# Performance work log

Measured on AMD Instinct MI355X. Metric: run time of the kernel, lower is better.

## Reference

```python
import jax, jax.numpy as jnp
import numpy as np

TEMPERATURE = 0.1
NSAMPLE = 32
B, N_PER, M_PER, C_FEAT = 2, 16384, 4096, 64


def setup_inputs() -> dict:
    key = jax.random.key(0)
    ks = jax.random.split(key, 4)
    xyz = jax.random.normal(ks[0], (B * N_PER, 3), jnp.float32)
    new_xyz = jax.random.normal(ks[1], (B * M_PER, 3), jnp.float32)
    new_xyz_r = jax.random.uniform(ks[2], (B * M_PER, 1), jnp.float32, minval=0.5, maxval=1.0)
    features = jax.random.normal(ks[3], (B * N_PER, C_FEAT), jnp.float32)
    xyz_batch_cnt = jnp.full((B,), N_PER, jnp.int32)
    new_xyz_batch_cnt = jnp.full((B,), M_PER, jnp.int32)
    temperature_decay = jnp.ones((1,), jnp.float32)
    return dict(xyz=xyz, xyz_batch_cnt=xyz_batch_cnt, new_xyz=new_xyz,
                new_xyz_r=new_xyz_r, new_xyz_batch_cnt=new_xyz_batch_cnt,
                features=features, temperature_decay=temperature_decay)


def _ball_query(xyz_b, new_xyz_b, r_b, nsample):
    # xyz_b: (B,N,3), new_xyz_b: (B,M,3), r_b: (B,M)
    # Returns idx (B,M,nsample) int32 (batch-local point indices, first-in-order
    # within the ball, remaining slots filled with first hit, 0 if empty) and
    # empty mask (B,M) bool. Mirrors the CUDA ball_query_deform kernel.
    N = xyz_b.shape[1]
    d2 = jnp.sum((new_xyz_b[:, :, None, :] - xyz_b[:, None, :, :]) ** 2, axis=-1)  # (B,M,N)
    within = d2 < (r_b ** 2)[..., None]
    # key = point index if within radius else N; top_k of -key gives the first
    # nsample in-ball indices in ascending index order.
    key = jnp.where(within, jnp.arange(N, dtype=jnp.int32), jnp.int32(N))
    neg_vals, _ = jax.lax.top_k(-key, nsample)
    cand = -neg_vals  # (B,M,nsample)
    cnt = within.sum(axis=-1)  # (B,M)
    slot_valid = jnp.arange(nsample) < cnt[..., None]
    idx = jnp.where(slot_valid, cand, cand[..., :1])  # pad with first found index
    empty = cnt == 0
    idx = jnp.where(empty[..., None], 0, idx)
    return idx.astype(jnp.int32), empty


def reference(xyz, xyz_batch_cnt, new_xyz, new_xyz_r, new_xyz_batch_cnt, features, temperature_decay):
    b = xyz_batch_cnt.shape[0]
    n = xyz.shape[0] // b
    m = new_xyz.shape[0] // b
    c = features.shape[1]
    real_t = TEMPERATURE * temperature_decay[0]
    explore_r = new_xyz_r + real_t * 5.0  # (M_tot, 1)

    xyz_b = xyz.reshape(b, n, 3)
    nxyz_b = new_xyz.reshape(b, m, 3)
    idx_b, empty_b = _ball_query(xyz_b, nxyz_b, explore_r.reshape(b, m), NSAMPLE)

    gather = jax.vmap(lambda pts, i: pts[i])  # per-batch gather

    grouped_xyz = gather(xyz_b, idx_b)                 # (B,M,ns,3)
    grouped_xyz = grouped_xyz - nxyz_b[:, :, None, :]  # center
    grouped_xyz = jnp.where(empty_b[:, :, None, None], 0.0, grouped_xyz)
    grouped_xyz = grouped_xyz.reshape(b * m, NSAMPLE, 3).transpose(0, 2, 1)  # (M_tot,3,ns)

    dist_xyz = jnp.sqrt(jnp.sum(grouped_xyz * grouped_xyz, axis=1))  # (M_tot,ns)
    weights = 1.0 - jax.nn.sigmoid((dist_xyz - new_xyz_r) / real_t)  # (M_tot,ns)

    feat_b = features.reshape(b, n, c)
    grouped_feat = gather(feat_b, idx_b)  # (B,M,ns,C)
    grouped_feat = jnp.where(empty_b[:, :, None, None], 0.0, grouped_feat)
    grouped_feat = grouped_feat.reshape(b * m, NSAMPLE, c).transpose(0, 2, 1)  # (M_tot,C,ns)

    new_features = jnp.concatenate([grouped_xyz, grouped_feat], axis=1)  # (M_tot,3+C,ns)
    idx = idx_b.reshape(b * m, NSAMPLE)
    return new_features, weights, idx
```

## Files before the change

### kernel.cpp

```cpp
#include <hip/hip_runtime.h>
#include <math.h>

#define NS 32
#define WPB 4
#define SCAN0 2048
#define TSTRIDE 36

__device__ __forceinline__ void write_query(
    int m, int bb, bool empty, int lane,
    const int* sIdxW, float* sT,
    const float* __restrict__ xyz, const float* __restrict__ new_xyz,
    const float* __restrict__ new_xyz_r, const float* __restrict__ features,
    float real_t, float* __restrict__ out, int N_per, int C, int M_tot)
{
#pragma clang fp contract(off)
    const float* xb = xyz + (size_t)bb * N_per * 3;
    const int    j  = lane & 31;
    const size_t nf_base = (size_t)m * (3 + C) * NS;
    float* wout = out + (size_t)M_tot * (3 + C) * NS;
    float* iout = wout + (size_t)M_tot * NS;

    if (lane < NS) {
        const float qx = new_xyz[(size_t)m * 3 + 0];
        const float qy = new_xyz[(size_t)m * 3 + 1];
        const float qz = new_xyz[(size_t)m * 3 + 2];
        const float r_orig = new_xyz_r[m];
        const int pj = empty ? 0 : sIdxW[j];
        float gx = 0.f, gy = 0.f, gz = 0.f;
        if (!empty) {
            gx = xb[(size_t)pj * 3 + 0] - qx;
            gy = xb[(size_t)pj * 3 + 1] - qy;
            gz = xb[(size_t)pj * 3 + 2] - qz;
        }
        float d2 = gx * gx;
        d2 = d2 + gy * gy;
        d2 = d2 + gz * gz;
        float dist = sqrtf(d2);
        float wt = 1.0f / (1.0f + expf((dist - r_orig) / real_t));
        out[nf_base + 0 * NS + j] = gx;
        out[nf_base + 1 * NS + j] = gy;
        out[nf_base + 2 * NS + j] = gz;
        wout[(size_t)m * NS + j] = wt;
        iout[(size_t)m * NS + j] = (float)pj;
    }

    const float* fb = features + (size_t)bb * N_per * C;
    int c0 = 0;
    for (; c0 + 32 <= C; c0 += 32) {
        const int k  = lane & 7;
        const int f4 = 4 * (k & 3);
        #pragma unroll
        for (int t = 0; t < 4; ++t) {
            const int r  = 8 * t + (lane >> 3);
            const int pj = empty ? 0 : sIdxW[r];
            float4 v = make_float4(0.f, 0.f, 0.f, 0.f);
            if (!empty) v = *(const float4*)(fb + (size_t)pj * C + c0 + 4 * k);
            const int rs = r ^ f4;
            sT[(4 * k + 0) * TSTRIDE + rs] = v.x;
            sT[(4 * k + 1) * TSTRIDE + rs] = v.y;
            sT[(4 * k + 2) * TSTRIDE + rs] = v.z;
            sT[(4 * k + 3) * TSTRIDE + rs] = v.w;
        }
        const int jg = lane & 7;
        #pragma unroll
        for (int s2 = 0; s2 < 4; ++s2) {
            const int ch = 8 * s2 + (lane >> 3);
            const int jb = (4 * jg) ^ (4 * ((ch >> 2) & 3));
            float4 w = *(const float4*)&sT[ch * TSTRIDE + jb];
            *(float4*)&out[nf_base + (size_t)(3 + c0 + ch) * NS + 4 * jg] = w;
        }
    }
    if (c0 < C) {
        const int h  = lane >> 5;
        const int pj = empty ? 0 : sIdxW[j];
        const float* frow = fb + (size_t)pj * C;
        for (int c = c0 + h; c < C; c += 2) {
            float v = empty ? 0.f : frow[c];
            out[nf_base + (size_t)(3 + c) * NS + j] = v;
        }
    }
}

__global__ __launch_bounds__(256) void qgd_AC(
    const float* __restrict__ xyz, const float* __restrict__ new_xyz,
    const float* __restrict__ new_xyz_r, const float* __restrict__ features,
    const float* __restrict__ tdec, float* __restrict__ out,
    int* __restrict__ counter, int* __restrict__ list,
    int N_per, int M_per, int C, int M_tot)
{
#pragma clang fp contract(off)
    __shared__ __align__(16) float sBuf[WPB * 32 * TSTRIDE];
    __shared__ int sIdx[WPB][NS];

    const int lane = threadIdx.x & 63;
    const int wv   = threadIdx.x >> 6;
    const int m    = blockIdx.x * WPB + wv;
    if (m >= M_tot) return;

    const int bb = m / M_per;
    const float* xb = xyz + (size_t)bb * N_per * 3;
    const float qx = new_xyz[(size_t)m * 3 + 0];
    const float qy = new_xyz[(size_t)m * 3 + 1];
    const float qz = new_xyz[(size_t)m * 3 + 2];
    const float real_t = 0.1f * tdec[0];
    const float er  = new_xyz_r[m] + real_t * 5.0f;
    const float er2 = er * er;
    const unsigned long long lt = (1ull << lane) - 1ull;

    const int scan0 = (SCAN0 < N_per) ? SCAN0 : N_per;
    int cnt = 0;
    for (int base = 0; base < scan0; base += 256) {
        float d2k[4];
        #pragma unroll
        for (int k = 0; k < 4; ++k) {
            int p = base + k * 64 + lane;
            int pc = (p < N_per) ? p : (N_per - 1);
            const float* pp = xb + (size_t)pc * 3;
            float dx = pp[0] - qx, dy = pp[1] - qy, dz = pp[2] - qz;
            float d2 = dx * dx;
            d2 = d2 + dy * dy;
            d2 = d2 + dz * dz;
            d2k[k] = (p < N_per) ? d2 : 1e30f;
        }
        #pragma unroll
        for (int k = 0; k < 4; ++k) {
            bool hit = d2k[k] < er2;
            unsigned long long msk = __ballot(hit);
            if (hit) {
                int slot = cnt + (int)__popcll(msk & lt);
                if (slot < NS) sIdx[wv][slot] = base + k * 64 + lane;
            }
            cnt += (int)__popcll(msk);
        }
        if (cnt >= NS) break;
    }

    if (cnt >= NS) {
        write_query(m, bb, false, lane, sIdx[wv],
                    sBuf + wv * (32 * TSTRIDE),
                    xyz, new_xyz, new_xyz_r, features, real_t, out,
                    N_per, C, M_tot);
    } else if (lane == 0) {
        int pos = atomicAdd(counter, 1);
        list[pos] = m;
    }
}

__global__ __launch_bounds__(256) void qgd_B(
    const float* __restrict__ xyz, const float* __restrict__ new_xyz,
    const float* __restrict__ new_xyz_r, const float* __restrict__ features,
    const float* __restrict__ tdec, float* __restrict__ out,
    const int* __restrict__ counter, const int* __restrict__ list,
    int N_per, int M_per, int C, int M_tot)
{
#pragma clang fp contract(off)
    __shared__ int sH[WPB][NS];
    __shared__ int sC[WPB];
    __shared__ int sM[NS];
    __shared__ int sTot;
    __shared__ __align__(16) float sT[32 * TSTRIDE];

    const int lane = threadIdx.x & 63;
    const int wv   = threadIdx.x >> 6;
    const int nstrag = *counter;
    const unsigned long long lt = (1ull << lane) - 1ull;
    const float real_t = 0.1f * tdec[0];

    for (int it = blockIdx.x; it < nstrag; it += gridDim.x) {
        const int m  = list[it];
        const int bb = m / M_per;
        const float* xb = xyz + (size_t)bb * N_per * 3;
        const float qx = new_xyz[(size_t)m * 3 + 0];
        const float qy = new_xyz[(size_t)m * 3 + 1];
        const float qz = new_xyz[(size_t)m * 3 + 2];
        const float er  = new_xyz_r[m] + real_t * 5.0f;
        const float er2 = er * er;

        const int rb = (int)(((long long)N_per * wv) / WPB);
        const int re = (int)(((long long)N_per * (wv + 1)) / WPB);

        int cnt = 0;
        for (int base = rb; base < re; base += 256) {
            float d2k[4];
            #pragma unroll
            for (int k = 0; k < 4; ++k) {
                int p = base + k * 64 + lane;
                int pc = (p < re) ? p : (re - 1);
                const float* pp = xb + (size_t)pc * 3;
                float dx = pp[0] - qx, dy = pp[1] - qy, dz = pp[2] - qz;
                float d2 = dx * dx;
                d2 = d2 + dy * dy;
                d2 = d2 + dz * dz;
                d2k[k] = (p < re) ? d2 : 1e30f;
            }
            #pragma unroll
            for (int k = 0; k < 4; ++k) {
                bool hit = d2k[k] < er2;
                unsigned long long msk = __ballot(hit);
                if (hit) {
                    int slot = cnt + (int)__popcll(msk & lt);
                    if (slot < NS) sH[wv][slot] = base + k * 64 + lane;
                }
                cnt += (int)__popcll(msk);
            }
            if (cnt >= NS) break;
        }
        if (lane == 0) sC[wv] = (cnt < NS) ? cnt : NS;
        __syncthreads();

        if (threadIdx.x < NS) {
            const int j  = threadIdx.x;
            const int c0 = sC[0], c1 = sC[1], c2 = sC[2], c3 = sC[3];
            const int o1 = c0, o2 = c0 + c1, o3 = o2 + c2;
            const int tot = o3 + c3;
            int v = 0;
            if (j < tot) {
                if      (j >= o3) v = sH[3][j - o3];
                else if (j >= o2) v = sH[2][j - o2];
                else if (j >= o1) v = sH[1][j - o1];
                else              v = sH[0][j];
            }
            int first = 0;
            if      (c0 > 0) first = sH[0][0];
            else if (c1 > 0) first = sH[1][0];
            else if (c2 > 0) first = sH[2][0];
            else if (c3 > 0) first = sH[3][0];
            sM[j] = (tot == 0) ? 0 : ((j < tot) ? v : first);
            if (j == 0) sTot = tot;
        }
        __syncthreads();

        if (wv == 0) {
            write_query(m, bb, (sTot == 0), lane, sM, sT,
                        xyz, new_xyz, new_xyz_r, features, real_t, out,
                        N_per, C, M_tot);
        }
        __syncthreads();
    }
}

extern "C" void kernel_launch(void* const* d_in, const int* in_sizes, int n_in,
                              void* d_out, int out_size, void* d_ws, size_t ws_size,
                              hipStream_t stream) {
    const float* xyz       = (const float*)d_in[0];
    const float* new_xyz   = (const float*)d_in[2];
    const float* new_xyz_r = (const float*)d_in[3];
    const float* features  = (const float*)d_in[5];
    const float* tdec      = (const float*)d_in[6];

    const int B     = in_sizes[1];
    const int N_tot = in_sizes[0] / 3;
    const int M_tot = in_sizes[2] / 3;
    const int C     = in_sizes[5] / N_tot;
    const int N_per = N_tot / B;
    const int M_per = M_tot / B;

    float* out     = (float*)d_out;
    int*   counter = (int*)d_ws;
    int*   list    = (int*)d_ws + 4;

    hipMemsetAsync(counter, 0, sizeof(int), stream);

    const int blocksA = (M_tot + WPB - 1) / WPB;
    qgd_AC<<<blocksA, 256, 0, stream>>>(xyz, new_xyz, new_xyz_r, features,
                                        tdec, out, counter, list,
                                        N_per, M_per, C, M_tot);
    qgd_B<<<512, 256, 0, stream>>>(xyz, new_xyz, new_xyz_r, features,
                                   tdec, out, counter, list,
                                   N_per, M_per, C, M_tot);
}
```

Before: 122.9 us.

## Fuse straggler ball-query pass into main kernel with in-block cooperative rescan

Merges the two-kernel scheme (fast prefix scan plus a straggler list handled by a second kernel) into one kernel. Queries that do not find enough neighbours in the first 2048 points are now finished inside the same block: all four waves split only the remaining points and merge with the prefix hits. This removes the memset, the atomic list, the second launch, and the rescan of the already-scanned prefix. In exchange, a block with stragglers runs them one after another with block-wide syncs, which can leave waves idle and lengthen the tail.

```diff
diff --git a/kernel.cpp b/kernel.cpp
--- a/kernel.cpp
+++ b/kernel.cpp
@@ -81,94 +81,69 @@
     }
 }
 
-__global__ __launch_bounds__(256) void qgd_AC(
+__device__ __forceinline__ int scan_range(
+    const float* __restrict__ xb, float qx, float qy, float qz, float er2,
+    int rb, int re, int lane, unsigned long long lt, int* hits)
+{
+#pragma clang fp contract(off)
+    int cnt = 0;
+    for (int base = rb; base < re; base += 256) {
+        float d2k[4];
+        #pragma unroll
+        for (int k = 0; k < 4; ++k) {
+            int p = base + k * 64 + lane;
+            int pc = (p < re) ? p : (re - 1);
+            const float* pp = xb + (size_t)pc * 3;
+            float dx = pp[0] - qx, dy = pp[1] - qy, dz = pp[2] - qz;
+            float d2 = dx * dx;
+            d2 = d2 + dy * dy;
+            d2 = d2 + dz * dz;
+            d2k[k] = (p < re) ? d2 : 1e30f;
+        }
+        #pragma unroll
+        for (int k = 0; k < 4; ++k) {
+            bool hit = d2k[k] < er2;
+            unsigned long long msk = __ballot(hit);
+            if (hit) {
+                int slot = cnt + (int)__popcll(msk & lt);
+                if (slot < NS) hits[slot] = base + k * 64 + lane;
+            }
+            cnt += (int)__popcll(msk);
+        }
+        if (cnt >= NS) break;
+    }
+    return cnt;
+}
+
+__global__ __launch_bounds__(256) void qgd_F(
     const float* __restrict__ xyz, const float* __restrict__ new_xyz,
     const float* __restrict__ new_xyz_r, const float* __restrict__ features,
     const float* __restrict__ tdec, float* __restrict__ out,
-    int* __restrict__ counter, int* __restrict__ list,
     int N_per, int M_per, int C, int M_tot)
 {
 #pragma clang fp contract(off)
     __shared__ __align__(16) float sBuf[WPB * 32 * TSTRIDE];
     __shared__ int sIdx[WPB][NS];
+    __shared__ int sH[WPB][NS];
+    __shared__ int sCnt[WPB];
+    __shared__ int sStrag[WPB];
+    __shared__ int sC[WPB];
+    __shared__ int sM[NS];
+    __shared__ int sTot;
 
     const int lane = threadIdx.x & 63;
     const int wv   = threadIdx.x >> 6;
     const int m    = blockIdx.x * WPB + wv;
-    if (m >= M_tot) return;
-
-    const int bb = m / M_per;
-    const float* xb = xyz + (size_t)bb * N_per * 3;
-    const float qx = new_xyz[(size_t)m * 3 + 0];
-    const float qy = new_xyz[(size_t)m * 3 + 1];
-    const float qz = new_xyz[(size_t)m * 3 + 2];
+    const bool valid = (m < M_tot);
+
     const float real_t = 0.1f * tdec[0];
-    const float er  = new_xyz_r[m] + real_t * 5.0f;
-    const float er2 = er * er;
     const unsigned long long lt = (1ull << lane) - 1ull;
-
     const int scan0 = (SCAN0 < N_per) ? SCAN0 : N_per;
+
     int cnt = 0;
-    for (int base = 0; base < scan0; base += 256) {
-        float d2k[4];
-        #pragma unroll
-        for (int k = 0; k < 4; ++k) {
-            int p = base + k * 64 + lane;
-            int pc = (p < N_per) ? p : (N_per - 1);
-            const float* pp = xb + (size_t)pc * 3;
-            float dx = pp[0] - qx, dy = pp[1] - qy, dz = pp[2] - qz;
-            float d2 = dx * dx;
-            d2 = d2 + dy * dy;
-            d2 = d2 + dz * dz;
-            d2k[k] = (p < N_per) ? d2 : 1e30f;
-        }
-        #pragma unroll
-        for (int k = 0; k < 4; ++k) {
-            bool hit = d2k[k] < er2;
-            unsigned long long msk = __ballot(hit);
-            if (hit) {
-                int slot = cnt + (int)__popcll(msk & lt);
-                if (slot < NS) sIdx[wv][slot] = base + k * 64 + lane;
-            }
-            cnt += (int)__popcll(msk);
-        }
-        if (cnt >= NS) break;
-    }
-
-    if (cnt >= NS) {
-        write_query(m, bb, false, lane, sIdx[wv],
-                    sBuf + wv * (32 * TSTRIDE),
-                    xyz, new_xyz, new_xyz_r, features, real_t, out,
-                    N_per, C, M_tot);
-    } else if (lane == 0) {
-        int pos = atomicAdd(counter, 1);
-        list[pos] = m;
-    }
-}
-
-__global__ __launch_bounds__(256) void qgd_B(
-    const float* __restrict__ xyz, const float* __restrict__ new_xyz,
-    const float* __restrict__ new_xyz_r, const float* __restrict__ features,
-    const float* __restrict__ tdec, float* __restrict__ out,
-    const int* __restrict__ counter, const int* __restrict__ list,
-    int N_per, int M_per, int C, int M_tot)
-{
-#pragma clang fp contract(off)
-    __shared__ int sH[WPB][NS];
-    __shared__ int sC[WPB];
-    __shared__ int sM[NS];
-    __shared__ int sTot;
-    __shared__ __align__(16) float sT[32 * TSTRIDE];
-
-    const int lane = threadIdx.x & 63;
-    const int wv   = threadIdx.x >> 6;
-    const int nstrag = *counter;
-    const unsigned long long lt = (1ull << lane) - 1ull;
-    const float real_t = 0.1f * tdec[0];
-
-    for (int it = blockIdx.x; it < nstrag; it += gridDim.x) {
-        const int m  = list[it];
-        const int bb = m / M_per;
+    int bb = 0;
+    if (valid) {
+        bb = m / M_per;
         const float* xb = xyz + (size_t)bb * N_per * 3;
         const float qx = new_xyz[(size_t)m * 3 + 0];
         const float qy = new_xyz[(size_t)m * 3 + 1];
@@ -176,62 +151,68 @@
         const float er  = new_xyz_r[m] + real_t * 5.0f;
         const float er2 = er * er;
 
-        const int rb = (int)(((long long)N_per * wv) / WPB);
-        const int re = (int)(((long long)N_per * (wv + 1)) / WPB);
-
-        int cnt = 0;
-        for (int base = rb; base < re; base += 256) {
-            float d2k[4];
-            #pragma unroll
-            for (int k = 0; k < 4; ++k) {
-                int p = base + k * 64 + lane;
-                int pc = (p < re) ? p : (re - 1);
-                const float* pp = xb + (size_t)pc * 3;
-                float dx = pp[0] - qx, dy = pp[1] - qy, dz = pp[2] - qz;
-                float d2 = dx * dx;
-                d2 = d2 + dy * dy;
-                d2 = d2 + dz * dz;
-                d2k[k] = (p < re) ? d2 : 1e30f;
-            }
-            #pragma unroll
-            for (int k = 0; k < 4; ++k) {
-                bool hit = d2k[k] < er2;
-                unsigned long long msk = __ballot(hit);
-                if (hit) {
-                    int slot = cnt + (int)__popcll(msk & lt);
-                    if (slot < NS) sH[wv][slot] = base + k * 64 + lane;
-                }
-                cnt += (int)__popcll(msk);
-            }
-            if (cnt >= NS) break;
-        }
-        if (lane == 0) sC[wv] = (cnt < NS) ? cnt : NS;
+        cnt = scan_range(xb, qx, qy, qz, er2, 0, scan0, lane, lt, sIdx[wv]);
+
+        if (cnt >= NS) {
+            write_query(m, bb, false, lane, sIdx[wv],
+                        sBuf + wv * (32 * TSTRIDE),
+                        xyz, new_xyz, new_xyz_r, features, real_t, out,
+                        N_per, C, M_tot);
+        }
+    }
+    if (lane == 0) {
+        sCnt[wv]   = cnt;
+        sStrag[wv] = (valid && cnt < NS) ? 1 : 0;
+    }
+    __syncthreads();
+
+    for (int s = 0; s < WPB; ++s) {
+        if (!sStrag[s]) continue;
+
+        const int ms  = blockIdx.x * WPB + s;
+        const int bbs = ms / M_per;
+        const float* xbs = xyz + (size_t)bbs * N_per * 3;
+        const float qx = new_xyz[(size_t)ms * 3 + 0];
+        const float qy = new_xyz[(size_t)ms * 3 + 1];
+        const float qz = new_xyz[(size_t)ms * 3 + 2];
+        const float er  = new_xyz_r[ms] + real_t * 5.0f;
+        const float er2 = er * er;
+
+        const int rem = N_per - scan0;
+        const int rb  = scan0 + (int)(((long long)rem * wv) / WPB);
+        const int re  = scan0 + (int)(((long long)rem * (wv + 1)) / WPB);
+
+        int c2 = scan_range(xbs, qx, qy, qz, er2, rb, re, lane, lt, sH[wv]);
+        if (lane == 0) sC[wv] = (c2 < NS) ? c2 : NS;
         __syncthreads();
 
         if (threadIdx.x < NS) {
             const int j  = threadIdx.x;
-            const int c0 = sC[0], c1 = sC[1], c2 = sC[2], c3 = sC[3];
-            const int o1 = c0, o2 = c0 + c1, o3 = o2 + c2;
+            const int cp = sCnt[s];
+            const int c0 = sC[0], c1 = sC[1], c2_ = sC[2], c3 = sC[3];
+            const int o0 = cp, o1 = o0 + c0, o2 = o1 + c1, o3 = o2 + c2_;
             const int tot = o3 + c3;
             int v = 0;
             if (j < tot) {
-                if      (j >= o3) v = sH[3][j - o3];
-                else if (j >= o2) v = sH[2][j - o2];
-                else if (j >= o1) v = sH[1][j - o1];
-                else              v = sH[0][j];
+                if      (j <  o0) v = sIdx[s][j];
+                else if (j <  o1) v = sH[0][j - o0];
+                else if (j <  o2) v = sH[1][j - o1];
+                else if (j <  o3) v = sH[2][j - o2];
+                else              v = sH[3][j - o3];
             }
             int first = 0;
-            if      (c0 > 0) first = sH[0][0];
-            else if (c1 > 0) first = sH[1][0];
-            else if (c2 > 0) first = sH[2][0];
-            else if (c3 > 0) first = sH[3][0];
+            if      (cp  > 0) first = sIdx[s][0];
+            else if (c0  > 0) first = sH[0][0];
+            else if (c1  > 0) first = sH[1][0];
+            else if (c2_ > 0) first = sH[2][0];
+            else if (c3  > 0) first = sH[3][0];
             sM[j] = (tot == 0) ? 0 : ((j < tot) ? v : first);
             if (j == 0) sTot = tot;
         }
         __syncthreads();
 
         if (wv == 0) {
-            write_query(m, bb, (sTot == 0), lane, sM, sT,
+            write_query(ms, bbs, (sTot == 0), lane, sM, sBuf,
                         xyz, new_xyz, new_xyz_r, features, real_t, out,
                         N_per, C, M_tot);
         }
@@ -255,17 +236,9 @@
     const int N_per = N_tot / B;
     const int M_per = M_tot / B;
 
-    float* out     = (float*)d_out;
-    int*   counter = (int*)d_ws;
-    int*   list    = (int*)d_ws + 4;
-
-    hipMemsetAsync(counter, 0, sizeof(int), stream);
-
-    const int blocksA = (M_tot + WPB - 1) / WPB;
-    qgd_AC<<<blocksA, 256, 0, stream>>>(xyz, new_xyz, new_xyz_r, features,
-                                        tdec, out, counter, list,
-                                        N_per, M_per, C, M_tot);
-    qgd_B<<<512, 256, 0, stream>>>(xyz, new_xyz, new_xyz_r, features,
-                                   tdec, out, counter, list,
-                                   N_per, M_per, C, M_tot);
-}
+    float* out = (float*)d_out;
+
+    const int blocks = (M_tot + WPB - 1) / WPB;
+    qgd_F<<<blocks, 256, 0, stream>>>(xyz, new_xyz, new_xyz_r, features,
+                                      tdec, out, N_per, M_per, C, M_tot);
+}
```

After: 115.7 us. 5.9% less time.
